# Performance work log

Hardware: AMD Instinct MI355X
Metric: run time of the kernel (lower is better)

## Reference

```python
import jax, jax.numpy as jnp
import numpy as np
import math

D = 256        # input_size == d_k == d_v (per the module: d_k = input_size)
H = 4          # n_heads
MAX_LEN = 800  # PositionalEncoding max_len
NEG = float(-(2**32) + 1)
LN_EPS = 1e-5


def _make_pe():
    pe = np.zeros((MAX_LEN, D), dtype=np.float32)
    pos = np.arange(MAX_LEN, dtype=np.float32)[:, None]
    div = np.exp(np.arange(0, D, 2, dtype=np.float32) * -(math.log(10000.0) / D))
    pe[:, 0::2] = np.sin(pos * div)
    pe[:, 1::2] = np.cos(pos * div)
    return jnp.asarray(pe)


def setup_inputs() -> dict:
    key = jax.random.key(0)
    ks = jax.random.split(key, 12)
    B, L = 32, 512

    def xavier(k, shape):
        fan_in, fan_out = shape[0], shape[1]
        std = math.sqrt(2.0 / (fan_in + fan_out))
        return jax.random.normal(k, shape, dtype=jnp.float32) * std

    return {
        "Q": jax.random.normal(ks[0], (B, L, D), dtype=jnp.float32),
        "K": jax.random.normal(ks[1], (B, L, D), dtype=jnp.float32),
        "V": jax.random.normal(ks[2], (B, L, D), dtype=jnp.float32),
        "mask": jax.random.randint(ks[3], (B, L), 0, 2).astype(jnp.bool_),
        "pe": _make_pe(),
        "W_q": xavier(ks[4], (D, H * D)),
        "W_k": xavier(ks[5], (D, H * D)),
        "W_v": xavier(ks[6], (D, H * D)),
        "W_o": xavier(ks[7], (H * D, D)),
        "w1": xavier(ks[8], (D, D)),
        "b1": jnp.zeros((D,), dtype=jnp.float32),
        "w2": xavier(ks[9], (D, D)),
        "b2": jnp.zeros((D,), dtype=jnp.float32),
        "gamma": jnp.ones((D,), dtype=jnp.float32),
        "beta": jnp.zeros((D,), dtype=jnp.float32),
    }


def _layer_norm(x, gamma, beta):
    mu = jnp.mean(x, axis=-1, keepdims=True)
    var = jnp.mean(jnp.square(x - mu), axis=-1, keepdims=True)
    return (x - mu) * jax.lax.rsqrt(var + LN_EPS) * gamma + beta


def _mha(Q, K, V, mask, W_q, W_k, W_v, W_o):
    B, Lq, _ = Q.shape
    Lk = K.shape[1]

    def split_heads(X, W, L):
        # (B, L, D) @ (D, H*D) -> (B*H, L, D)
        return (X @ W).reshape(B, L, H, D).transpose(0, 2, 1, 3).reshape(B * H, L, D)

    Qh = split_heads(Q, W_q, Lq)
    Kh = split_heads(K, W_k, Lk)
    Vh = split_heads(V, W_v, Lk)

    scale = D ** 0.5 + 1e-6
    scores = jnp.einsum('bqd,bkd->bqk', Qh, Kh) / scale  # (B*H, Lq, Lk)

    pad = jnp.broadcast_to(mask[:, None, :], (B, H, Lq)).reshape(B * H, Lq)
    pad_mask = jnp.broadcast_to(pad[:, :, None], (B * H, Lq, Lk))
    causal = jnp.triu(jnp.ones((Lq, Lk), dtype=jnp.bool_), k=1)
    full_mask = causal[None] | pad_mask
    scores = jnp.where(full_mask, NEG, scores)

    att = jax.nn.softmax(scores, axis=-1)
    Vatt = jnp.einsum('bqk,bkd->bqd', att, Vh)  # (B*H, Lq, D)
    Vatt = Vatt.reshape(B, H, Lq, D).transpose(0, 2, 1, 3).reshape(B, Lq, H * D)
    return Vatt @ W_o


def reference(Q, K, V, mask, pe, W_q, W_k, W_v, W_o, w1, b1, w2, b2, gamma, beta):
    Lq, Lk, Lv = Q.shape[1], K.shape[1], V.shape[1]
    Qp = Q + pe[None, :Lq]
    Kp = K + pe[None, :Lk]
    Vp = V + pe[None, :Lv]

    Vatt = _mha(Qp, Kp, Vp, mask, W_q, W_k, W_v, W_o)
    X = _layer_norm(Qp + Vatt, gamma, beta)
    ffn = jax.nn.relu(X @ w1.T + b1) @ w2.T + b2
    return _layer_norm(ffn + X, gamma, beta)
```

## Files before the change

kernel.cpp:

```cpp
#include <hip/hip_runtime.h>
#include <stdint.h>

#define SEQ   512
#define DM    256
#define NB    32
#define NH    4
#define HD    (NH * DM)
#define PE_MASK (SEQ * DM - 1)
#define NEGV  (-4294967295.0f)

typedef __attribute__((ext_vector_type(8))) short short8;
typedef __attribute__((ext_vector_type(4))) float f32x4;

#if defined(__has_builtin)
#if __has_builtin(__builtin_amdgcn_global_load_lds)
#define HAS_ASYNC 1
#endif
#endif
#ifndef HAS_ASYNC
#define HAS_ASYNC 0
#endif

__device__ __forceinline__ float b2f(unsigned short u) {
    return __uint_as_float(((uint32_t)u) << 16);
}
__device__ __forceinline__ unsigned short f2b(float f) {
    uint32_t u = __float_as_uint(f);
    u += 0x7fffu + ((u >> 16) & 1u);
    return (unsigned short)(u >> 16);
}
__device__ __forceinline__ float fast_exp2(float x) {
    float r;
    asm("v_exp_f32 %0, %1" : "=v"(r) : "v"(x));
    return r;
}

__device__ __forceinline__ int swzb(int b) {
    return b ^ (((b >> 7) & 7) << 4);
}

__global__ __launch_bounds__(256) void mask_canon(
    const unsigned char* __restrict__ raw, int* __restrict__ canon)
{
    __shared__ int enc_byte, enc_odd;
    int tid = threadIdx.x;
    if (tid == 0) { enc_byte = 0; enc_odd = 0; }
    __syncthreads();
    if (tid < 255 && raw[tid * 4 + 1]) atomicOr(&enc_byte, 1);
    if (tid < 128 && ((const int*)raw)[tid * 2 + 1]) atomicOr(&enc_odd, 1);
    __syncthreads();
    int i = blockIdx.x * 256 + tid;
    int v;
    if (enc_byte)      v = (raw[i] != 0);
    else if (enc_odd)  v = (((const int*)raw)[i] != 0);
    else               v = ((((const int*)raw)[i * 2] | ((const int*)raw)[i * 2 + 1]) != 0);
    canon[i] = v;
}

__global__ __launch_bounds__(256) void addpe3(
    const float* __restrict__ Q, const float* __restrict__ K,
    const float* __restrict__ V, const float* __restrict__ pe,
    unsigned short* __restrict__ Qp, unsigned short* __restrict__ Kp,
    unsigned short* __restrict__ Vp)
{
    int blk = blockIdx.x;
    int seg = blk >> 12;
    const float* X = (seg == 0) ? Q : (seg == 1) ? K : V;
    unsigned short* O = (seg == 0) ? Qp : (seg == 1) ? Kp : Vp;
    long i = (long)((blk & 4095) * 256 + threadIdx.x) * 4;
    float4 x = *reinterpret_cast<const float4*>(X + i);
    float4 p = *reinterpret_cast<const float4*>(pe + (i & PE_MASK));
    ushort4 o;
    o.x = f2b(x.x + p.x); o.y = f2b(x.y + p.y);
    o.z = f2b(x.z + p.z); o.w = f2b(x.w + p.w);
    *reinterpret_cast<ushort4*>(O + i) = o;
}

__global__ __launch_bounds__(256) void conv2(
    const float* __restrict__ w1, const float* __restrict__ w2,
    unsigned short* __restrict__ o1, unsigned short* __restrict__ o2)
{
    int blk = blockIdx.x;
    const float* in = (blk < 64) ? w1 : w2;
    unsigned short* out = (blk < 64) ? o1 : o2;
    long i = (long)((blk & 63) * 256 + threadIdx.x) * 4;
    float4 x = *reinterpret_cast<const float4*>(in + i);
    ushort4 o;
    o.x = f2b(x.x); o.y = f2b(x.y); o.z = f2b(x.z); o.w = f2b(x.w);
    *reinterpret_cast<ushort4*>(out + i) = o;
}

__global__ __launch_bounds__(256) void transpose_f2b3(
    const float* __restrict__ in0, const float* __restrict__ in1,
    const float* __restrict__ in2, unsigned short* __restrict__ out,
    int ldin, int ldout, long outStride)
{
    int z = blockIdx.z;
    const float* in = (z == 0) ? in0 : (z == 1) ? in1 : in2;
    unsigned short* op = out + z * outStride;
    __shared__ unsigned short tile[32][33];
    int r0 = blockIdx.y * 32, c0 = blockIdx.x * 32;
    int i = threadIdx.x >> 3;
    int j = (threadIdx.x & 7) * 4;
    float4 v = *reinterpret_cast<const float4*>(in + (long)(r0 + i) * ldin + c0 + j);
    tile[i][j + 0] = f2b(v.x); tile[i][j + 1] = f2b(v.y);
    tile[i][j + 2] = f2b(v.z); tile[i][j + 3] = f2b(v.w);
    __syncthreads();
    ushort4 w;
    w.x = tile[j + 0][i]; w.y = tile[j + 1][i]; w.z = tile[j + 2][i]; w.w = tile[j + 3][i];
    *reinterpret_cast<ushort4*>(op + (long)(c0 + i) * ldout + r0 + j) = w;
}

__global__ __launch_bounds__(256) void transpose_f2b(
    const float* __restrict__ in, unsigned short* __restrict__ out,
    int ldin, int ldout)
{
    __shared__ unsigned short tile[32][33];
    int r0 = blockIdx.y * 32, c0 = blockIdx.x * 32;
    int i = threadIdx.x >> 3;
    int j = (threadIdx.x & 7) * 4;
    float4 v = *reinterpret_cast<const float4*>(in + (long)(r0 + i) * ldin + c0 + j);
    tile[i][j + 0] = f2b(v.x); tile[i][j + 1] = f2b(v.y);
    tile[i][j + 2] = f2b(v.z); tile[i][j + 3] = f2b(v.w);
    __syncthreads();
    ushort4 w;
    w.x = tile[j + 0][i]; w.y = tile[j + 1][i]; w.z = tile[j + 2][i]; w.w = tile[j + 3][i];
    *reinterpret_cast<ushort4*>(out + (long)(c0 + i) * ldout + r0 + j) = w;
}

__global__ __launch_bounds__(256) void transpose_bf16(
    const unsigned short* __restrict__ in, unsigned short* __restrict__ out,
    int ldin, int ldout, long sInB, long sInH, long sOutB, long sOutH, int Hdiv)
{
    int z = blockIdx.z; int b = z / Hdiv; int h = z % Hdiv;
    const unsigned short* ip = in + b * sInB + h * sInH;
    unsigned short* op = out + b * sOutB + h * sOutH;
    __shared__ unsigned short tile[32][33];
    int r0 = blockIdx.y * 32, c0 = blockIdx.x * 32;
    int i = threadIdx.x >> 3;
    int j = (threadIdx.x & 7) * 4;
    ushort4 v = *reinterpret_cast<const ushort4*>(ip + (long)(r0 + i) * ldin + c0 + j);
    tile[i][j + 0] = v.x; tile[i][j + 1] = v.y; tile[i][j + 2] = v.z; tile[i][j + 3] = v.w;
    __syncthreads();
    ushort4 w;
    w.x = tile[j + 0][i]; w.y = tile[j + 1][i]; w.z = tile[j + 2][i]; w.w = tile[j + 3][i];
    *reinterpret_cast<ushort4*>(op + (long)(c0 + i) * ldout + r0 + j) = w;
}

__global__ __launch_bounds__(256) void vmean_part(
    const unsigned short* __restrict__ Vh, float* __restrict__ part)
{
    int bl = blockIdx.x, seg = blockIdx.y;
    const unsigned short* p = Vh + (long)bl * SEQ * HD + (long)seg * 64 * HD;
    int c = threadIdx.x * 4;
    float s0 = 0.f, s1 = 0.f, s2 = 0.f, s3 = 0.f;
    for (int l = 0; l < 64; ++l) {
        ushort4 v = *reinterpret_cast<const ushort4*>(p + (long)l * HD + c);
        s0 += b2f(v.x); s1 += b2f(v.y); s2 += b2f(v.z); s3 += b2f(v.w);
    }
    float4 o = {s0, s1, s2, s3};
    *reinterpret_cast<float4*>(part + (long)(bl * 8 + seg) * HD + c) = o;
}

__global__ __launch_bounds__(256) void vmean_reduce(
    const float* __restrict__ part, unsigned short* __restrict__ Vm)
{
    int bl = blockIdx.x;
    int c = threadIdx.x * 4;
    const float* p = part + (long)bl * 8 * HD + c;
    float s0 = 0.f, s1 = 0.f, s2 = 0.f, s3 = 0.f;
#pragma unroll
    for (int seg = 0; seg < 8; ++seg) {
        float4 v = *reinterpret_cast<const float4*>(p + (long)seg * HD);
        s0 += v.x; s1 += v.y; s2 += v.z; s3 += v.w;
    }
    const float inv = 1.0f / SEQ;
    ushort4 o;
    o.x = f2b(s0 * inv); o.y = f2b(s1 * inv);
    o.z = f2b(s2 * inv); o.w = f2b(s3 * inv);
    *reinterpret_cast<ushort4*>(Vm + (long)bl * HD + c) = o;
}

__global__ __launch_bounds__(256) void fix_mask(
    const unsigned short* __restrict__ Vm, unsigned short* __restrict__ Vatt,
    const int* __restrict__ maskc, int b0)
{
    int row = blockIdx.x * 4 + (threadIdx.x >> 6);
    int bl = row >> 9, l = row & (SEQ - 1);
    if (maskc[(long)(b0 + bl) * SEQ + l] == 0) return;
    int c = (threadIdx.x & 63) * 16;
    uint4 a = *reinterpret_cast<const uint4*>(Vm + (long)bl * HD + c);
    uint4 b = *reinterpret_cast<const uint4*>(Vm + (long)bl * HD + c + 8);
    *reinterpret_cast<uint4*>(Vatt + (long)row * HD + c) = a;
    *reinterpret_cast<uint4*>(Vatt + (long)row * HD + c + 8) = b;
}

template<bool BIAS, bool RELU, bool OUTBF16>
__global__ __launch_bounds__(256) void gemm_bt(
    const unsigned short* __restrict__ A, int lda,
    const unsigned short* __restrict__ B, int ldb,
    void* __restrict__ Cv, int ldc,
    const float* __restrict__ bias, float scale, int K, int Hdiv,
    long sAb, long sAh, long sAz,
    long sBb, long sBh, long sBz,
    long sCb, long sCh, long sCz)
{
    const int m0 = blockIdx.y * 128;
    const int n0 = blockIdx.x * 128;
    int z  = blockIdx.z;
    int bb = z / Hdiv, hh = z % Hdiv;
    const unsigned short* Ab = A + bb * sAb + hh * sAh + (long)z * sAz;
    const unsigned short* Bb = B + bb * sBb + hh * sBh + (long)z * sBz;
    long coff = bb * sCb + hh * sCh + (long)z * sCz;
    const float scl = (z == 0) ? scale : 1.0f;

    __shared__ unsigned short As[128 * 32];
    __shared__ unsigned short Bs[128 * 32];

    const int tid  = threadIdx.x;
    const int lane = tid & 63;
    const int wave = tid >> 6;
    const int wm   = (wave >> 1) * 64;
    const int wn   = (wave & 1) * 64;
    const int lm   = lane & 15;
    const int kq   = (lane >> 4) * 8;

    f32x4 acc[4][4] = {};

    for (int k0 = 0; k0 < K; k0 += 32) {
#pragma unroll
        for (int it = 0; it < 2; ++it) {
            int id = tid + it * 256;
            int r  = id >> 2;
            int c8 = (id & 3) * 8;
            const unsigned short* gA = Ab + (long)(m0 + r) * lda + k0 + c8;
            const unsigned short* gB = Bb + (long)(n0 + r) * ldb + k0 + c8;
#if HAS_ASYNC
            unsigned short* lA = &As[(size_t)(it * 256 + wave * 64) * 8];
            unsigned short* lB = &Bs[(size_t)(it * 256 + wave * 64) * 8];
            __builtin_amdgcn_global_load_lds(
                (const __attribute__((address_space(1))) void*)gA,
                (__attribute__((address_space(3))) void*)lA, 16, 0, 0);
            __builtin_amdgcn_global_load_lds(
                (const __attribute__((address_space(1))) void*)gB,
                (__attribute__((address_space(3))) void*)lB, 16, 0, 0);
#else
            *reinterpret_cast<uint4*>(&As[(size_t)id * 8]) =
                *reinterpret_cast<const uint4*>(gA);
            *reinterpret_cast<uint4*>(&Bs[(size_t)id * 8]) =
                *reinterpret_cast<const uint4*>(gB);
#endif
        }
        __syncthreads();

        short8 af[4], bfr[4];
#pragma unroll
        for (int i = 0; i < 4; ++i)
            af[i] = *reinterpret_cast<const short8*>(&As[(wm + i * 16 + lm) * 32 + kq]);
#pragma unroll
        for (int j = 0; j < 4; ++j)
            bfr[j] = *reinterpret_cast<const short8*>(&Bs[(wn + j * 16 + lm) * 32 + kq]);
#pragma unroll
        for (int i = 0; i < 4; ++i)
#pragma unroll
            for (int j = 0; j < 4; ++j)
                acc[i][j] = __builtin_amdgcn_mfma_f32_16x16x32_bf16(af[i], bfr[j], acc[i][j], 0, 0, 0);
        __syncthreads();
    }

#pragma unroll
    for (int j = 0; j < 4; ++j) {
        int col  = n0 + wn + j * 16 + lm;
        float bv = 0.f;
        if (BIAS) bv = bias[col];
#pragma unroll
        for (int i = 0; i < 4; ++i) {
#pragma unroll
            for (int r = 0; r < 4; ++r) {
                int row = m0 + wm + i * 16 + (lane >> 4) * 4 + r;
                float v = acc[i][j][r] * scl + bv;
                if (RELU) v = fmaxf(v, 0.f);
                long idx = coff + (long)row * ldc + col;
                if (OUTBF16) reinterpret_cast<unsigned short*>(Cv)[idx] = f2b(v);
                else         reinterpret_cast<float*>(Cv)[idx] = v;
            }
        }
    }
}

__device__ __forceinline__ void stage_k32(
    unsigned short* __restrict__ buf, const unsigned short* __restrict__ Ak,
    int kc, int qt, int tid, int wave)
{
    for (int it = 0; it <= qt; ++it) {
        int id = tid + it * 256;
#if HAS_ASYNC
        int U = swzb(id * 16);
        const unsigned short* g = Ak + (long)(U >> 6) * HD + kc * 32 + ((U >> 4) & 3) * 8;
        unsigned short* l = buf + (size_t)(it * 256 + wave * 64) * 8;
        __builtin_amdgcn_global_load_lds(
            (const __attribute__((address_space(1))) void*)g,
            (__attribute__((address_space(3))) void*)l, 16, 0, 0);
#else
        const unsigned short* g = Ak + (long)(id >> 2) * HD + kc * 32 + (id & 3) * 8;
        *reinterpret_cast<uint4*>((char*)buf + swzb(id * 16)) =
            *reinterpret_cast<const uint4*>(g);
#endif
    }
}

__device__ __forceinline__ void stage_v64(
    unsigned short* __restrict__ buf, const unsigned short* __restrict__ Av,
    int c64, int tid, int wave)
{
#pragma unroll
    for (int it = 0; it < 8; ++it) {
        int id = tid + it * 256;
#if HAS_ASYNC
        int U = swzb(id * 16);
        const unsigned short* g = Av + (long)(U >> 7) * SEQ + c64 * 64 + ((U >> 4) & 7) * 8;
        unsigned short* l = buf + (size_t)(it * 256 + wave * 64) * 8;
        __builtin_amdgcn_global_load_lds(
            (const __attribute__((address_space(1))) void*)g,
            (__attribute__((address_space(3))) void*)l, 16, 0, 0);
#else
        const unsigned short* g = Av + (long)(id >> 3) * SEQ + c64 * 64 + (id & 7) * 8;
        *reinterpret_cast<uint4*>((char*)buf + swzb(id * 16)) =
            *reinterpret_cast<const uint4*>(g);
#endif
    }
}

__global__ __launch_bounds__(256, 2) void flash_attn(
    const unsigned short* __restrict__ Qh,
    const unsigned short* __restrict__ Kh,
    const unsigned short* __restrict__ VhT,
    unsigned short* __restrict__ Vatt,
    const int* __restrict__ maskc, int bh0, int nbh)
{
    const int tid  = threadIdx.x;
    const int lane = tid & 63;
    const int wave = tid >> 6;
    const int lm   = lane & 15;
    const int qg   = lane >> 4;
    const int kq   = qg * 8;

    const int L = blockIdx.x;
    int z, qt;
    if ((nbh & 7) == 0) {
        int x = L & 7, m = L >> 3;
        int mq = m & 7;
        qt = (mq & 1) ? (7 - (mq >> 1)) : (mq >> 1);
        z  = x + 8 * (m >> 3);
    } else {
        z = L % nbh; qt = L / nbh;
    }
    const int b_l = z >> 2, h = z & 3;
    const int m0  = qt * 64;
    const int wq0 = m0 + wave * 16;
    const long qkbase = (long)b_l * SEQ * HD + (long)h * DM;
    const unsigned short* Aq = Qh + qkbase;
    const unsigned short* Ak = Kh + qkbase;
    const unsigned short* Av = VhT + (long)b_l * SEQ * HD + (long)h * SEQ * DM;
    unsigned short* Ov = Vatt + qkbase;
    const int bglob = (bh0 + z) >> 2;

    __shared__ unsigned short Ks[2 * SEQ * 32];
    __shared__ __align__(16) unsigned short Pw[4][16][40];

    f32x4 S[32] = {};
    const int NT = (m0 >> 4) + wave + 1;

    stage_k32(Ks, Ak, 0, qt, tid, wave);
    __syncthreads();
    for (int kc = 0; kc < 8; ++kc) {
        unsigned short* cur = (kc & 1) ? (Ks + SEQ * 32) : Ks;
        unsigned short* nxt = (kc & 1) ? Ks : (Ks + SEQ * 32);
        short8 qf = *reinterpret_cast<const short8*>(
            Aq + (long)(wq0 + lm) * HD + kc * 32 + kq);
        if (kc < 7) {
            stage_k32(nxt, Ak, kc + 1, qt, tid, wave);
        } else {
            stage_v64(Ks, Av, 0, tid, wave);
        }
        __builtin_amdgcn_s_setprio(1);
#pragma unroll
        for (int nt = 0; nt < 32; ++nt) {
            if (nt < NT) {
                int row = nt * 16 + lm;
                short8 bf = *reinterpret_cast<const short8*>(
                    (const char*)cur + swzb(row * 64 + qg * 16));
                S[nt] = __builtin_amdgcn_mfma_f32_16x16x32_bf16(qf, bf, S[nt], 0, 0, 0);
            }
        }
        __builtin_amdgcn_s_setprio(0);
        __syncthreads();
    }

    int   qrow[4];
    bool  rowm[4];
    float mx[4], sm[4];
#pragma unroll
    for (int r = 0; r < 4; ++r) {
        int q = wq0 + qg * 4 + r;
        qrow[r] = q;
        rowm[r] = maskc[bglob * SEQ + q] != 0;
        mx[r] = -3.4e38f;
    }
#pragma unroll
    for (int nt = 0; nt < 32; ++nt) {
        int k = nt * 16 + lm;
#pragma unroll
        for (int r = 0; r < 4; ++r) {
            float v = S[nt][r];
            if (k > qrow[r]) v = NEGV;
            S[nt][r] = v;
            mx[r] = fmaxf(mx[r], v);
        }
    }
#pragma unroll
    for (int r = 0; r < 4; ++r) {
#pragma unroll
        for (int off = 8; off >= 1; off >>= 1)
            mx[r] = fmaxf(mx[r], __shfl_xor(mx[r], off));
        sm[r] = 0.f;
    }
    uint32_t pk[32][2];
#pragma unroll
    for (int nt = 0; nt < 32; ++nt) {
        float e0 = fast_exp2(S[nt][0] - mx[0]);
        float e1 = fast_exp2(S[nt][1] - mx[1]);
        float e2 = fast_exp2(S[nt][2] - mx[2]);
        float e3 = fast_exp2(S[nt][3] - mx[3]);
        sm[0] += e0; sm[1] += e1; sm[2] += e2; sm[3] += e3;
        pk[nt][0] = (uint32_t)f2b(e0) | ((uint32_t)f2b(e1) << 16);
        pk[nt][1] = (uint32_t)f2b(e2) | ((uint32_t)f2b(e3) << 16);
    }
#pragma unroll
    for (int r = 0; r < 4; ++r) {
#pragma unroll
        for (int off = 8; off >= 1; off >>= 1)
            sm[r] += __shfl_xor(sm[r], off);
        sm[r] = 1.0f / sm[r];
    }

    unsigned short* Vb0 = Ks;
    unsigned short* Vb1 = Ks + 16384;
    const int NC = qt + 1;
    f32x4 O[16] = {};
#pragma unroll
    for (int c64 = 0; c64 < 8; ++c64) {
        if (c64 < NC) {
            unsigned short* Vcur = (c64 & 1) ? Vb1 : Vb0;
            __syncthreads();
            if (c64 + 1 < NC) {
                unsigned short* Vnext = (c64 & 1) ? Vb0 : Vb1;
                stage_v64(Vnext, Av, c64 + 1, tid, wave);
            }
#pragma unroll
            for (int t = 0; t < 2; ++t) {
#pragma unroll
                for (int tt = 0; tt < 2; ++tt) {
                    int nt = c64 * 4 + t * 2 + tt;
#pragma unroll
                    for (int r = 0; r < 4; ++r)
                        Pw[wave][qg * 4 + r][tt * 16 + lm] =
                            (unsigned short)(pk[nt][r >> 1] >> ((r & 1) * 16));
                }
                short8 pf = *reinterpret_cast<const short8*>(&Pw[wave][lm][kq]);
                __builtin_amdgcn_s_setprio(1);
#pragma unroll
                for (int nt2 = 0; nt2 < 16; ++nt2) {
                    int row = nt2 * 16 + lm;
                    short8 vf = *reinterpret_cast<const short8*>(
                        (const char*)Vcur + swzb(row * 128 + t * 64 + qg * 16));
                    O[nt2] = __builtin_amdgcn_mfma_f32_16x16x32_bf16(pf, vf, O[nt2], 0, 0, 0);
                }
                __builtin_amdgcn_s_setprio(0);
            }
        }
    }

#pragma unroll
    for (int nt2 = 0; nt2 < 16; ++nt2) {
#pragma unroll
        for (int r = 0; r < 4; ++r) {
            if (!rowm[r]) {
                int l = wq0 + qg * 4 + r;
                Ov[(long)l * HD + nt2 * 16 + lm] = f2b(O[nt2][r] * sm[r]);
            }
        }
    }
}

__global__ __launch_bounds__(256) void ln1_kernel(
    const unsigned short* __restrict__ AttO, const float* __restrict__ Q,
    const float* __restrict__ pe,
    const float* __restrict__ gamma, const float* __restrict__ beta,
    float* __restrict__ outf, unsigned short* __restrict__ outb)
{
    int row  = blockIdx.x * 4 + (threadIdx.x >> 6);
    int lane = threadIdx.x & 63;
    long base = (long)row * DM + lane * 4;
    ushort4 a = *reinterpret_cast<const ushort4*>(AttO + base);
    float4 qv = *reinterpret_cast<const float4*>(Q + base);
    float4 pv = *reinterpret_cast<const float4*>(pe + (base & PE_MASK));
    float x[4] = {b2f(a.x) + qv.x + pv.x, b2f(a.y) + qv.y + pv.y,
                  b2f(a.z) + qv.z + pv.z, b2f(a.w) + qv.w + pv.w};
    float s = x[0] + x[1] + x[2] + x[3];
#pragma unroll
    for (int off = 32; off > 0; off >>= 1) s += __shfl_xor(s, off);
    float mu = s * (1.0f / DM);
    float vs = 0.f;
#pragma unroll
    for (int t = 0; t < 4; ++t) { float d = x[t] - mu; vs += d * d; }
#pragma unroll
    for (int off = 32; off > 0; off >>= 1) vs += __shfl_xor(vs, off);
    float inv = rsqrtf(vs * (1.0f / DM) + 1e-5f);
    int d0 = lane * 4;
    float4 g = *reinterpret_cast<const float4*>(gamma + d0);
    float4 bt = *reinterpret_cast<const float4*>(beta + d0);
    float4 o;
    o.x = (x[0] - mu) * inv * g.x + bt.x;
    o.y = (x[1] - mu) * inv * g.y + bt.y;
    o.z = (x[2] - mu) * inv * g.z + bt.z;
    o.w = (x[3] - mu) * inv * g.w + bt.w;
    *reinterpret_cast<float4*>(outf + base) = o;
    ushort4 ob;
    ob.x = f2b(o.x); ob.y = f2b(o.y); ob.z = f2b(o.z); ob.w = f2b(o.w);
    *reinterpret_cast<ushort4*>(outb + base) = ob;
}

__global__ __launch_bounds__(256) void ln2_kernel(
    const float* __restrict__ F, const float* __restrict__ X,
    const float* __restrict__ gamma, const float* __restrict__ beta,
    float* __restrict__ out)
{
    int row  = blockIdx.x * 4 + (threadIdx.x >> 6);
    int lane = threadIdx.x & 63;
    long base = (long)row * DM + lane * 4;
    float4 a = *reinterpret_cast<const float4*>(F + base);
    float4 c = *reinterpret_cast<const float4*>(X + base);
    float x[4] = {a.x + c.x, a.y + c.y, a.z + c.z, a.w + c.w};
    float s = x[0] + x[1] + x[2] + x[3];
#pragma unroll
    for (int off = 32; off > 0; off >>= 1) s += __shfl_xor(s, off);
    float mu = s * (1.0f / DM);
    float vs = 0.f;
#pragma unroll
    for (int t = 0; t < 4; ++t) { float d = x[t] - mu; vs += d * d; }
#pragma unroll
    for (int off = 32; off > 0; off >>= 1) vs += __shfl_xor(vs, off);
    float inv = rsqrtf(vs * (1.0f / DM) + 1e-5f);
    int d0 = lane * 4;
    float4 g = *reinterpret_cast<const float4*>(gamma + d0);
    float4 bt = *reinterpret_cast<const float4*>(beta + d0);
    float4 o;
    o.x = (x[0] - mu) * inv * g.x + bt.x;
    o.y = (x[1] - mu) * inv * g.y + bt.y;
    o.z = (x[2] - mu) * inv * g.z + bt.z;
    o.w = (x[3] - mu) * inv * g.w + bt.w;
    *reinterpret_cast<float4*>(out + base) = o;
}

extern "C" void kernel_launch(void* const* d_in, const int* in_sizes, int n_in,
                              void* d_out, int out_size, void* d_ws, size_t ws_size,
                              hipStream_t stream)
{
    const float* Q  = (const float*)d_in[0];
    const float* Ki = (const float*)d_in[1];
    const float* Vi = (const float*)d_in[2];
    const unsigned char* mask_raw = (const unsigned char*)d_in[3];
    const float* pe = (const float*)d_in[4];
    const float* Wq = (const float*)d_in[5];
    const float* Wk = (const float*)d_in[6];
    const float* Wv = (const float*)d_in[7];
    const float* Wo = (const float*)d_in[8];
    const float* w1 = (const float*)d_in[9];
    const float* b1 = (const float*)d_in[10];
    const float* w2 = (const float*)d_in[11];
    const float* b2 = (const float*)d_in[12];
    const float* gamma = (const float*)d_in[13];
    const float* beta  = (const float*)d_in[14];
    float* out = (float*)d_out;

    const size_t MiB = 1048576;
    char* ws = (char*)d_ws;

    int CB = 1;
    for (int cb = 32; cb >= 1; cb >>= 1) {
        size_t scr_sz = (size_t)(5 * cb) * MiB + (size_t)cb * 34816;
        if (scr_sz < 24 * MiB) scr_sz = 24 * MiB;
        if ((59 * MiB + scr_sz) <= ws_size) { CB = cb; break; }
    }
    const int NCH = NB / CB;

    unsigned short* WqT  = (unsigned short*)(ws);
    unsigned short* WkT  = WqT + 262144;
    unsigned short* WvT  = WkT + 262144;
    unsigned short* WoT  = WvT + 262144;
    unsigned short* w1b  = (unsigned short*)(ws + 2 * MiB);
    unsigned short* w2b  = w1b + 65536;
    int*            maskc = (int*)(ws + 2 * MiB + 262144);
    unsigned short* Qp   = (unsigned short*)(ws + 3 * MiB);
    unsigned short* Kp   = (unsigned short*)(ws + 11 * MiB);
    unsigned short* Vp   = (unsigned short*)(ws + 19 * MiB);
    unsigned short* AttO = (unsigned short*)(ws + 27 * MiB);
    unsigned short* Xb   = (unsigned short*)(ws + 35 * MiB);
    float*          Xf   = (float*)(ws + 43 * MiB);
    char*           scr  = ws + 59 * MiB;
    unsigned short* Qh   = (unsigned short*)(scr);
    unsigned short* Kh   = (unsigned short*)(scr + (size_t)CB * MiB);
    unsigned short* Vh   = (unsigned short*)(scr + (size_t)2 * CB * MiB);
    unsigned short* VhT  = (unsigned short*)(scr + (size_t)3 * CB * MiB);
    unsigned short* Vatt = (unsigned short*)(scr + (size_t)4 * CB * MiB);
    float*          part = (float*)(scr + (size_t)5 * CB * MiB);
    unsigned short* Vm   = (unsigned short*)(scr + (size_t)5 * CB * MiB
                                             + (size_t)CB * 8 * HD * 4);
    unsigned short* H1   = (unsigned short*)(scr);
    float*          Ff   = (float*)(scr + 8 * MiB);

    const float SCALE_Q = (float)((1.0 / (16.0 + 1e-6)) * 1.4426950408889634);
    const long CROWS = (long)CB * SEQ;
    const long CBELT = (long)CB * MiB / 2;

    mask_canon<<<64, 256, 0, stream>>>(mask_raw, maskc);
    transpose_f2b3<<<dim3(32, 8, 3), 256, 0, stream>>>(Wq, Wk, Wv, WqT, HD, DM, 262144);
    transpose_f2b<<<dim3(8, 32, 1), 256, 0, stream>>>(Wo, WoT, DM, HD);
    conv2<<<128, 256, 0, stream>>>(w1, w2, w1b, w2b);
    addpe3<<<12288, 256, 0, stream>>>(Q, Ki, Vi, pe, Qp, Kp, Vp);

    for (int c = 0; c < NCH; ++c) {
        const long r0   = (long)c * CROWS;
        const int  bh0  = c * CB * NH;
        const int  gy   = (int)(CROWS / 128);
        const int  nbh  = CB * NH;

        gemm_bt<false, false, true><<<dim3(8, gy, 3), 256, 0, stream>>>(
            Qp + r0 * DM, DM, WqT, DM, Qh, HD, nullptr, SCALE_Q, DM,
            1, 4194304, 0, 0, 262144, 0, 0, CBELT, 0, 0);

        transpose_bf16<<<dim3(8, 16, CB * NH), 256, 0, stream>>>(
            Vh, VhT, HD, SEQ, (long)SEQ * HD, DM, (long)SEQ * HD, (long)SEQ * DM, NH);

        vmean_part<<<dim3(CB, 8), 256, 0, stream>>>(Vh, part);
        vmean_reduce<<<CB, 256, 0, stream>>>(part, Vm);

        flash_attn<<<dim3(8 * nbh, 1, 1), 256, 0, stream>>>(
            Qh, Kh, VhT, Vatt, maskc, bh0, nbh);

        fix_mask<<<(int)(CROWS / 4), 256, 0, stream>>>(Vm, Vatt, maskc, c * CB);

        gemm_bt<false, false, true><<<dim3(2, gy, 1), 256, 0, stream>>>(
            Vatt, HD, WoT, HD, AttO + r0 * DM, DM, nullptr, 1.f, HD,
            1, 0,0,0, 0,0,0, 0,0,0);
    }

    ln1_kernel<<<4096, 256, 0, stream>>>(AttO, Q, pe, gamma, beta, Xf, Xb);

    gemm_bt<true, true, true><<<dim3(2, 128, 1), 256, 0, stream>>>(
        Xb, DM, w1b, DM, H1, DM, b1, 1.f, DM, 1, 0,0,0, 0,0,0, 0,0,0);
    gemm_bt<true, false, false><<<dim3(2, 128, 1), 256, 0, stream>>>(
        H1, DM, w2b, DM, Ff, DM, b2, 1.f, DM, 1, 0,0,0, 0,0,0, 0,0,0);

    ln2_kernel<<<4096, 256, 0, stream>>>(Ff, Xf, gamma, beta, out);
}
```

Measured before the change: 345.9 us.

## Fuse prep kernels, merge V transpose with mean, fold mask fill into attention

```diff
diff --git a/kernel.cpp b/kernel.cpp
--- a/kernel.cpp
+++ b/kernel.cpp
@@ -39,160 +39,125 @@
     return b ^ (((b >> 7) & 7) << 4);
 }
 
-__global__ __launch_bounds__(256) void mask_canon(
-    const unsigned char* __restrict__ raw, int* __restrict__ canon)
-{
-    __shared__ int enc_byte, enc_odd;
-    int tid = threadIdx.x;
-    if (tid == 0) { enc_byte = 0; enc_odd = 0; }
-    __syncthreads();
-    if (tid < 255 && raw[tid * 4 + 1]) atomicOr(&enc_byte, 1);
-    if (tid < 128 && ((const int*)raw)[tid * 2 + 1]) atomicOr(&enc_odd, 1);
-    __syncthreads();
-    int i = blockIdx.x * 256 + tid;
-    int v;
-    if (enc_byte)      v = (raw[i] != 0);
-    else if (enc_odd)  v = (((const int*)raw)[i] != 0);
-    else               v = ((((const int*)raw)[i * 2] | ((const int*)raw)[i * 2 + 1]) != 0);
-    canon[i] = v;
-}
-
-__global__ __launch_bounds__(256) void addpe3(
+__global__ __launch_bounds__(256) void prep_all(
+    const unsigned char* __restrict__ mask_raw, int* __restrict__ maskc,
+    const float* __restrict__ Wq, const float* __restrict__ Wk,
+    const float* __restrict__ Wv, unsigned short* __restrict__ WqT,
+    const float* __restrict__ Wo, unsigned short* __restrict__ WoT,
+    const float* __restrict__ w1, const float* __restrict__ w2,
+    unsigned short* __restrict__ o1, unsigned short* __restrict__ o2,
     const float* __restrict__ Q, const float* __restrict__ K,
     const float* __restrict__ V, const float* __restrict__ pe,
     unsigned short* __restrict__ Qp, unsigned short* __restrict__ Kp,
     unsigned short* __restrict__ Vp)
 {
-    int blk = blockIdx.x;
-    int seg = blk >> 12;
-    const float* X = (seg == 0) ? Q : (seg == 1) ? K : V;
-    unsigned short* O = (seg == 0) ? Qp : (seg == 1) ? Kp : Vp;
-    long i = (long)((blk & 4095) * 256 + threadIdx.x) * 4;
-    float4 x = *reinterpret_cast<const float4*>(X + i);
-    float4 p = *reinterpret_cast<const float4*>(pe + (i & PE_MASK));
-    ushort4 o;
-    o.x = f2b(x.x + p.x); o.y = f2b(x.y + p.y);
-    o.z = f2b(x.z + p.z); o.w = f2b(x.w + p.w);
-    *reinterpret_cast<ushort4*>(O + i) = o;
-}
-
-__global__ __launch_bounds__(256) void conv2(
-    const float* __restrict__ w1, const float* __restrict__ w2,
-    unsigned short* __restrict__ o1, unsigned short* __restrict__ o2)
-{
-    int blk = blockIdx.x;
-    const float* in = (blk < 64) ? w1 : w2;
-    unsigned short* out = (blk < 64) ? o1 : o2;
-    long i = (long)((blk & 63) * 256 + threadIdx.x) * 4;
-    float4 x = *reinterpret_cast<const float4*>(in + i);
-    ushort4 o;
-    o.x = f2b(x.x); o.y = f2b(x.y); o.z = f2b(x.z); o.w = f2b(x.w);
-    *reinterpret_cast<ushort4*>(out + i) = o;
-}
-
-__global__ __launch_bounds__(256) void transpose_f2b3(
-    const float* __restrict__ in0, const float* __restrict__ in1,
-    const float* __restrict__ in2, unsigned short* __restrict__ out,
-    int ldin, int ldout, long outStride)
-{
-    int z = blockIdx.z;
-    const float* in = (z == 0) ? in0 : (z == 1) ? in1 : in2;
-    unsigned short* op = out + z * outStride;
     __shared__ unsigned short tile[32][33];
-    int r0 = blockIdx.y * 32, c0 = blockIdx.x * 32;
-    int i = threadIdx.x >> 3;
-    int j = (threadIdx.x & 7) * 4;
-    float4 v = *reinterpret_cast<const float4*>(in + (long)(r0 + i) * ldin + c0 + j);
-    tile[i][j + 0] = f2b(v.x); tile[i][j + 1] = f2b(v.y);
-    tile[i][j + 2] = f2b(v.z); tile[i][j + 3] = f2b(v.w);
-    __syncthreads();
-    ushort4 w;
-    w.x = tile[j + 0][i]; w.y = tile[j + 1][i]; w.z = tile[j + 2][i]; w.w = tile[j + 3][i];
-    *reinterpret_cast<ushort4*>(op + (long)(c0 + i) * ldout + r0 + j) = w;
-}
-
-__global__ __launch_bounds__(256) void transpose_f2b(
-    const float* __restrict__ in, unsigned short* __restrict__ out,
-    int ldin, int ldout)
+    __shared__ int enc[2];
+    const int blk = blockIdx.x;
+    const int tid = threadIdx.x;
+
+    if (blk < 64) {
+        if (tid == 0) { enc[0] = 0; enc[1] = 0; }
+        __syncthreads();
+        if (tid < 255 && mask_raw[tid * 4 + 1]) atomicOr(&enc[0], 1);
+        if (tid < 128 && ((const int*)mask_raw)[tid * 2 + 1]) atomicOr(&enc[1], 1);
+        __syncthreads();
+        int i = blk * 256 + tid;
+        int v;
+        if (enc[0])      v = (mask_raw[i] != 0);
+        else if (enc[1]) v = (((const int*)mask_raw)[i] != 0);
+        else             v = ((((const int*)mask_raw)[i * 2] |
+                              ((const int*)mask_raw)[i * 2 + 1]) != 0);
+        maskc[i] = v;
+    } else if (blk < 832) {
+        int t = blk - 64;
+        int x = t & 31, y = (t >> 5) & 7, zz = t >> 8;
+        const float* in = (zz == 0) ? Wq : (zz == 1) ? Wk : Wv;
+        unsigned short* op = WqT + (long)zz * 262144;
+        int r0 = y * 32, c0 = x * 32;
+        int i = tid >> 3, j = (tid & 7) * 4;
+        float4 v = *reinterpret_cast<const float4*>(in + (long)(r0 + i) * HD + c0 + j);
+        tile[i][j + 0] = f2b(v.x); tile[i][j + 1] = f2b(v.y);
+        tile[i][j + 2] = f2b(v.z); tile[i][j + 3] = f2b(v.w);
+        __syncthreads();
+        ushort4 w;
+        w.x = tile[j + 0][i]; w.y = tile[j + 1][i];
+        w.z = tile[j + 2][i]; w.w = tile[j + 3][i];
+        *reinterpret_cast<ushort4*>(op + (long)(c0 + i) * DM + r0 + j) = w;
+    } else if (blk < 1088) {
+        int t = blk - 832;
+        int x = t & 7, y = t >> 3;
+        int r0 = y * 32, c0 = x * 32;
+        int i = tid >> 3, j = (tid & 7) * 4;
+        float4 v = *reinterpret_cast<const float4*>(Wo + (long)(r0 + i) * DM + c0 + j);
+        tile[i][j + 0] = f2b(v.x); tile[i][j + 1] = f2b(v.y);
+        tile[i][j + 2] = f2b(v.z); tile[i][j + 3] = f2b(v.w);
+        __syncthreads();
+        ushort4 w;
+        w.x = tile[j + 0][i]; w.y = tile[j + 1][i];
+        w.z = tile[j + 2][i]; w.w = tile[j + 3][i];
+        *reinterpret_cast<ushort4*>(WoT + (long)(c0 + i) * HD + r0 + j) = w;
+    } else if (blk < 1216) {
+        int t = blk - 1088;
+        const float* in = (t < 64) ? w1 : w2;
+        unsigned short* out = (t < 64) ? o1 : o2;
+        long i = (long)((t & 63) * 256 + tid) * 4;
+        float4 x = *reinterpret_cast<const float4*>(in + i);
+        ushort4 o;
+        o.x = f2b(x.x); o.y = f2b(x.y); o.z = f2b(x.z); o.w = f2b(x.w);
+        *reinterpret_cast<ushort4*>(out + i) = o;
+    } else {
+        int t = blk - 1216;
+        int seg = t >> 12;
+        const float* X = (seg == 0) ? Q : (seg == 1) ? K : V;
+        unsigned short* O = (seg == 0) ? Qp : (seg == 1) ? Kp : Vp;
+        long i = (long)((t & 4095) * 256 + tid) * 4;
+        float4 x = *reinterpret_cast<const float4*>(X + i);
+        float4 p = *reinterpret_cast<const float4*>(pe + (i & PE_MASK));
+        ushort4 o;
+        o.x = f2b(x.x + p.x); o.y = f2b(x.y + p.y);
+        o.z = f2b(x.z + p.z); o.w = f2b(x.w + p.w);
+        *reinterpret_cast<ushort4*>(O + i) = o;
+    }
+}
+
+__global__ __launch_bounds__(256) void tv_kernel(
+    const unsigned short* __restrict__ Vh, unsigned short* __restrict__ VhT,
+    float* __restrict__ part, int nbl)
 {
     __shared__ unsigned short tile[32][33];
-    int r0 = blockIdx.y * 32, c0 = blockIdx.x * 32;
-    int i = threadIdx.x >> 3;
-    int j = (threadIdx.x & 7) * 4;
-    float4 v = *reinterpret_cast<const float4*>(in + (long)(r0 + i) * ldin + c0 + j);
-    tile[i][j + 0] = f2b(v.x); tile[i][j + 1] = f2b(v.y);
-    tile[i][j + 2] = f2b(v.z); tile[i][j + 3] = f2b(v.w);
-    __syncthreads();
-    ushort4 w;
-    w.x = tile[j + 0][i]; w.y = tile[j + 1][i]; w.z = tile[j + 2][i]; w.w = tile[j + 3][i];
-    *reinterpret_cast<ushort4*>(out + (long)(c0 + i) * ldout + r0 + j) = w;
-}
-
-__global__ __launch_bounds__(256) void transpose_bf16(
-    const unsigned short* __restrict__ in, unsigned short* __restrict__ out,
-    int ldin, int ldout, long sInB, long sInH, long sOutB, long sOutH, int Hdiv)
-{
-    int z = blockIdx.z; int b = z / Hdiv; int h = z % Hdiv;
-    const unsigned short* ip = in + b * sInB + h * sInH;
-    unsigned short* op = out + b * sOutB + h * sOutH;
-    __shared__ unsigned short tile[32][33];
-    int r0 = blockIdx.y * 32, c0 = blockIdx.x * 32;
-    int i = threadIdx.x >> 3;
-    int j = (threadIdx.x & 7) * 4;
-    ushort4 v = *reinterpret_cast<const ushort4*>(ip + (long)(r0 + i) * ldin + c0 + j);
-    tile[i][j + 0] = v.x; tile[i][j + 1] = v.y; tile[i][j + 2] = v.z; tile[i][j + 3] = v.w;
-    __syncthreads();
-    ushort4 w;
-    w.x = tile[j + 0][i]; w.y = tile[j + 1][i]; w.z = tile[j + 2][i]; w.w = tile[j + 3][i];
-    *reinterpret_cast<ushort4*>(op + (long)(c0 + i) * ldout + r0 + j) = w;
-}
-
-__global__ __launch_bounds__(256) void vmean_part(
-    const unsigned short* __restrict__ Vh, float* __restrict__ part)
-{
-    int bl = blockIdx.x, seg = blockIdx.y;
-    const unsigned short* p = Vh + (long)bl * SEQ * HD + (long)seg * 64 * HD;
-    int c = threadIdx.x * 4;
-    float s0 = 0.f, s1 = 0.f, s2 = 0.f, s3 = 0.f;
-    for (int l = 0; l < 64; ++l) {
-        ushort4 v = *reinterpret_cast<const ushort4*>(p + (long)l * HD + c);
-        s0 += b2f(v.x); s1 += b2f(v.y); s2 += b2f(v.z); s3 += b2f(v.w);
-    }
-    float4 o = {s0, s1, s2, s3};
-    *reinterpret_cast<float4*>(part + (long)(bl * 8 + seg) * HD + c) = o;
-}
-
-__global__ __launch_bounds__(256) void vmean_reduce(
-    const float* __restrict__ part, unsigned short* __restrict__ Vm)
-{
-    int bl = blockIdx.x;
-    int c = threadIdx.x * 4;
-    const float* p = part + (long)bl * 8 * HD + c;
-    float s0 = 0.f, s1 = 0.f, s2 = 0.f, s3 = 0.f;
-#pragma unroll
-    for (int seg = 0; seg < 8; ++seg) {
-        float4 v = *reinterpret_cast<const float4*>(p + (long)seg * HD);
-        s0 += v.x; s1 += v.y; s2 += v.z; s3 += v.w;
-    }
-    const float inv = 1.0f / SEQ;
-    ushort4 o;
-    o.x = f2b(s0 * inv); o.y = f2b(s1 * inv);
-    o.z = f2b(s2 * inv); o.w = f2b(s3 * inv);
-    *reinterpret_cast<ushort4*>(Vm + (long)bl * HD + c) = o;
-}
-
-__global__ __launch_bounds__(256) void fix_mask(
-    const unsigned short* __restrict__ Vm, unsigned short* __restrict__ Vatt,
-    const int* __restrict__ maskc, int b0)
-{
-    int row = blockIdx.x * 4 + (threadIdx.x >> 6);
-    int bl = row >> 9, l = row & (SEQ - 1);
-    if (maskc[(long)(b0 + bl) * SEQ + l] == 0) return;
-    int c = (threadIdx.x & 63) * 16;
-    uint4 a = *reinterpret_cast<const uint4*>(Vm + (long)bl * HD + c);
-    uint4 b = *reinterpret_cast<const uint4*>(Vm + (long)bl * HD + c + 8);
-    *reinterpret_cast<uint4*>(Vatt + (long)row * HD + c) = a;
-    *reinterpret_cast<uint4*>(Vatt + (long)row * HD + c + 8) = b;
+    const int blk = blockIdx.x;
+    const int tid = threadIdx.x;
+    const int nT = nbl * NH * 128;
+
+    if (blk < nT) {
+        int x = blk & 7, y = (blk >> 3) & 15, zz = blk >> 7;
+        int b = zz / NH, hh = zz % NH;
+        const unsigned short* ip = Vh + (long)b * SEQ * HD + (long)hh * DM;
+        unsigned short* op = VhT + (long)b * SEQ * HD + (long)hh * SEQ * DM;
+        int r0 = y * 32, c0 = x * 32;
+        int i = tid >> 3, j = (tid & 7) * 4;
+        ushort4 v = *reinterpret_cast<const ushort4*>(ip + (long)(r0 + i) * HD + c0 + j);
+        tile[i][j + 0] = v.x; tile[i][j + 1] = v.y;
+        tile[i][j + 2] = v.z; tile[i][j + 3] = v.w;
+        __syncthreads();
+        ushort4 w;
+        w.x = tile[j + 0][i]; w.y = tile[j + 1][i];
+        w.z = tile[j + 2][i]; w.w = tile[j + 3][i];
+        *reinterpret_cast<ushort4*>(op + (long)(c0 + i) * SEQ + r0 + j) = w;
+    } else {
+        int t = blk - nT;
+        int bl = t >> 3, seg = t & 7;
+        const unsigned short* p = Vh + (long)bl * SEQ * HD + (long)seg * 64 * HD;
+        int c = tid * 4;
+        float s0 = 0.f, s1 = 0.f, s2 = 0.f, s3 = 0.f;
+        for (int l = 0; l < 64; ++l) {
+            ushort4 v = *reinterpret_cast<const ushort4*>(p + (long)l * HD + c);
+            s0 += b2f(v.x); s1 += b2f(v.y); s2 += b2f(v.z); s3 += b2f(v.w);
+        }
+        float4 o = {s0, s1, s2, s3};
+        *reinterpret_cast<float4*>(part + (long)(bl * 8 + seg) * HD + c) = o;
+    }
 }
 
 template<bool BIAS, bool RELU, bool OUTBF16>
@@ -335,6 +300,7 @@
     const unsigned short* __restrict__ Qh,
     const unsigned short* __restrict__ Kh,
     const unsigned short* __restrict__ VhT,
+    const float* __restrict__ part,
     unsigned short* __restrict__ Vatt,
     const int* __restrict__ maskc, int bh0, int nbh)
 {
@@ -481,14 +447,23 @@
         }
     }
 
+    const float* pb = part + (long)(b_l * 8) * HD + h * DM + lm;
+    float vmf[16];
 #pragma unroll
     for (int nt2 = 0; nt2 < 16; ++nt2) {
+        float s = 0.f;
+#pragma unroll
+        for (int seg = 0; seg < 8; ++seg)
+            s += pb[(long)seg * HD + nt2 * 16];
+        vmf[nt2] = s * (1.0f / SEQ);
+    }
+#pragma unroll
+    for (int nt2 = 0; nt2 < 16; ++nt2) {
 #pragma unroll
         for (int r = 0; r < 4; ++r) {
-            if (!rowm[r]) {
-                int l = wq0 + qg * 4 + r;
-                Ov[(long)l * HD + nt2 * 16 + lm] = f2b(O[nt2][r] * sm[r]);
-            }
+            int l = wq0 + qg * 4 + r;
+            float val = rowm[r] ? vmf[nt2] : O[nt2][r] * sm[r];
+            Ov[(long)l * HD + nt2 * 16 + lm] = f2b(val);
         }
     }
 }
@@ -589,7 +564,7 @@
 
     int CB = 1;
     for (int cb = 32; cb >= 1; cb >>= 1) {
-        size_t scr_sz = (size_t)(5 * cb) * MiB + (size_t)cb * 34816;
+        size_t scr_sz = (size_t)(5 * cb) * MiB + (size_t)cb * 32768;
         if (scr_sz < 24 * MiB) scr_sz = 24 * MiB;
         if ((59 * MiB + scr_sz) <= ws_size) { CB = cb; break; }
     }
@@ -615,8 +590,6 @@
     unsigned short* VhT  = (unsigned short*)(scr + (size_t)3 * CB * MiB);
     unsigned short* Vatt = (unsigned short*)(scr + (size_t)4 * CB * MiB);
     float*          part = (float*)(scr + (size_t)5 * CB * MiB);
-    unsigned short* Vm   = (unsigned short*)(scr + (size_t)5 * CB * MiB
-                                             + (size_t)CB * 8 * HD * 4);
     unsigned short* H1   = (unsigned short*)(scr);
     float*          Ff   = (float*)(scr + 8 * MiB);
 
@@ -624,11 +597,9 @@
     const long CROWS = (long)CB * SEQ;
     const long CBELT = (long)CB * MiB / 2;
 
-    mask_canon<<<64, 256, 0, stream>>>(mask_raw, maskc);
-    transpose_f2b3<<<dim3(32, 8, 3), 256, 0, stream>>>(Wq, Wk, Wv, WqT, HD, DM, 262144);
-    transpose_f2b<<<dim3(8, 32, 1), 256, 0, stream>>>(Wo, WoT, DM, HD);
-    conv2<<<128, 256, 0, stream>>>(w1, w2, w1b, w2b);
-    addpe3<<<12288, 256, 0, stream>>>(Q, Ki, Vi, pe, Qp, Kp, Vp);
+    prep_all<<<13504, 256, 0, stream>>>(
+        mask_raw, maskc, Wq, Wk, Wv, WqT, Wo, WoT,
+        w1, w2, w1b, w2b, Q, Ki, Vi, pe, Qp, Kp, Vp);
 
     for (int c = 0; c < NCH; ++c) {
         const long r0   = (long)c * CROWS;
@@ -640,16 +611,11 @@
             Qp + r0 * DM, DM, WqT, DM, Qh, HD, nullptr, SCALE_Q, DM,
             1, 4194304, 0, 0, 262144, 0, 0, CBELT, 0, 0);
 
-        transpose_bf16<<<dim3(8, 16, CB * NH), 256, 0, stream>>>(
-            Vh, VhT, HD, SEQ, (long)SEQ * HD, DM, (long)SEQ * HD, (long)SEQ * DM, NH);
-
-        vmean_part<<<dim3(CB, 8), 256, 0, stream>>>(Vh, part);
-        vmean_reduce<<<CB, 256, 0, stream>>>(part, Vm);
+        tv_kernel<<<CB * NH * 128 + CB * 8, 256, 0, stream>>>(
+            Vh, VhT, part, CB);
 
         flash_attn<<<dim3(8 * nbh, 1, 1), 256, 0, stream>>>(
-            Qh, Kh, VhT, Vatt, maskc, bh0, nbh);
-
-        fix_mask<<<(int)(CROWS / 4), 256, 0, stream>>>(Vm, Vatt, maskc, c * CB);
+            Qh, Kh, VhT, part, Vatt, maskc, bh0, nbh);
 
         gemm_bt<false, false, true><<<dim3(2, gy, 1), 256, 0, stream>>>(
             Vatt, HD, WoT, HD, AttO + r0 * DM, DM, nullptr, 1.f, HD,
```

Result: faster. 332.6 us (-3.8%).
